# Kernel tuning notes

Hardware: AMD Instinct MI355X
Metric: run time of the kernel (lower is better)

The kernel has to match this reference:

```python
import jax, jax.numpy as jnp
import numpy as np

B, D, DEPTH, H, E, N, NC = 128, 192, 12, 3, 4, 65, 100
WIN_HALF = 3  # window_size=7 -> |i-j| <= 3


def _ln(x, g, b, eps=1e-5):
    m = x.mean(-1, keepdims=True)
    v = ((x - m) ** 2).mean(-1, keepdims=True)
    return (x - m) / jnp.sqrt(v + eps) * g + b


def _forward(x, conv_w, conv_b, pe_g, pe_b, cls_token, pos_embed,
             n1_g, n1_b, qkv_w, temp, proj_w, proj_b, n2_g, n2_b,
             gate_w, gate_b, e_w1, e_b1, e_w2, e_b2, attn_scale, mlp_scale,
             norm_g, norm_b, hc_w, hc_b, head_w, head_b):
    Bx = x.shape[0]
    # patch embed: conv with kernel==stride==4 is a blocked matmul
    p = x.reshape(Bx, 3, 8, 4, 8, 4).transpose(0, 2, 4, 1, 3, 5).reshape(Bx, 64, 48)
    t = p @ conv_w.reshape(D, 48).T + conv_b
    t = _ln(t, pe_g, pe_b)
    t = jnp.concatenate([jnp.broadcast_to(cls_token, (Bx, 1, D)), t], axis=1) + pos_embed
    Nn = t.shape[1]
    hd = D // H
    scale = hd ** -0.5
    idx = jnp.arange(Nn)
    # local-window attention mask (log of {0,1} -> {-inf,0})
    mask = jnp.where(jnp.abs(idx[:, None] - idx[None, :]) <= WIN_HALF, 0.0, -jnp.inf)
    for l in range(DEPTH):
        # --- attention ---
        y = _ln(t, n1_g[l], n1_b[l])
        qkv = (y @ qkv_w[l].T).reshape(Bx, Nn, 3, H, hd).transpose(2, 0, 3, 1, 4)
        q, k, v = qkv[0], qkv[1], qkv[2]
        a = (q @ k.transpose(0, 1, 3, 2)) * scale / temp[l]  # [B,H,N,N]
        a = jax.nn.softmax(a + mask, axis=-1)
        o = (a @ v).transpose(0, 2, 1, 3).reshape(Bx, Nn, D)
        o = o @ proj_w[l].T + proj_b[l]
        t = t + attn_scale[l] * o
        # --- top-2 MoE (dense-equivalent of the masked per-expert dispatch) ---
        y = _ln(t, n2_g[l], n2_b[l])
        g = jax.nn.softmax(y @ gate_w[l].T + gate_b[l], axis=-1)  # [B,N,E]
        tg, ti = jax.lax.top_k(g, 2)
        tg = tg / tg.sum(-1, keepdims=True)
        h = jax.nn.gelu(jnp.einsum('bnc,ehc->bneh', y, e_w1[l]) + e_b1[l], approximate=False)
        eo = jnp.einsum('bneh,ech->bnec', h, e_w2[l]) + e_b2[l]  # [B,N,E,C]
        sel = jnp.take_along_axis(eo, ti[..., None], axis=2)  # [B,N,2,C]
        mo = (sel * tg[..., None]).sum(axis=2)
        t = t + mlp_scale[l] * mo
    t = _ln(t, norm_g, norm_b)
    cls = t[:, 0]
    # hypercomplex linear head: out[:,k] += x[:,j] @ W[(k-j)%n].T
    xv = cls.reshape(Bx, E, D // E)
    perm = (jnp.arange(E)[:, None] - jnp.arange(E)[None, :]) % E  # [k,j] -> i
    hh = jnp.einsum('bjc,kjoc->bko', xv, hc_w[perm]).reshape(Bx, 2 * D) + hc_b
    hh = jax.nn.gelu(hh, approximate=False)
    return hh @ head_w.T + head_b


def setup_inputs() -> dict:
    ks = iter(jax.random.split(jax.random.key(0), 64))
    def rn(shape, s=0.02):
        return jax.random.normal(next(ks), shape, jnp.float32) * s
    return dict(
        x=jax.random.normal(next(ks), (B, 3, 32, 32), jnp.float32),
        conv_w=rn((D, 3, 4, 4)), conv_b=jnp.zeros((D,)),
        pe_g=jnp.ones((D,)), pe_b=jnp.zeros((D,)),
        cls_token=rn((1, 1, D)), pos_embed=rn((1, N, D)),
        n1_g=jnp.ones((DEPTH, D)), n1_b=jnp.zeros((DEPTH, D)),
        qkv_w=rn((DEPTH, 3 * D, D)), temp=jnp.ones((DEPTH, H, 1, 1)),
        proj_w=rn((DEPTH, D, D)), proj_b=jnp.zeros((DEPTH, D)),
        n2_g=jnp.ones((DEPTH, D)), n2_b=jnp.zeros((DEPTH, D)),
        gate_w=rn((DEPTH, E, D)), gate_b=jnp.zeros((DEPTH, E)),
        e_w1=rn((DEPTH, E, 2 * D, D)), e_b1=jnp.zeros((DEPTH, E, 2 * D)),
        e_w2=rn((DEPTH, E, D, 2 * D)), e_b2=jnp.zeros((DEPTH, E, D)),
        attn_scale=jnp.ones((DEPTH,)), mlp_scale=jnp.ones((DEPTH,)),
        norm_g=jnp.ones((D,)), norm_b=jnp.zeros((D,)),
        hc_w=rn((E, 2 * D // E, D // E)), hc_b=jnp.zeros((2 * D,)),
        head_w=rn((NC, 2 * D)), head_b=jnp.zeros((NC,)),
    )


def reference(x, conv_w, conv_b, pe_g, pe_b, cls_token, pos_embed,
              n1_g, n1_b, qkv_w, temp, proj_w, proj_b, n2_g, n2_b,
              gate_w, gate_b, e_w1, e_b1, e_w2, e_b2, attn_scale, mlp_scale,
              norm_g, norm_b, hc_w, hc_b, head_w, head_b):
    return _forward(x, conv_w, conv_b, pe_g, pe_b, cls_token, pos_embed,
                    n1_g, n1_b, qkv_w, temp, proj_w, proj_b, n2_g, n2_b,
                    gate_w, gate_b, e_w1, e_b1, e_w2, e_b2, attn_scale, mlp_scale,
                    norm_g, norm_b, hc_w, hc_b, head_w, head_b)
```

## Files before the change

kernel.cpp:

```cpp
#include <hip/hip_runtime.h>
#include <cmath>

#define ROWS 8320
#define DD   192

typedef __attribute__((ext_vector_type(8))) _Float16 half8;
typedef __attribute__((ext_vector_type(4))) float floatx4;

#define GLD16(gp, lp) __builtin_amdgcn_global_load_lds( \
    (const __attribute__((address_space(1))) void*)(gp), \
    (__attribute__((address_space(3))) void*)(lp), 16, 0, 0)

#define MFMA_F16 __builtin_amdgcn_mfma_f32_16x16x32_f16

__device__ __forceinline__ float gelu_f(float x) {
    return 0.5f * x * (1.0f + erff(x * 0.70710678118654752440f));
}

__device__ __forceinline__ float blk_sum_192(float v, float* sbuf) {
    int tid = threadIdx.x;
    sbuf[tid] = v;
    __syncthreads();
    for (int off = 96; off >= 3; off >>= 1) {
        if (tid < off) sbuf[tid] += sbuf[tid + off];
        __syncthreads();
    }
    float r = sbuf[0] + sbuf[1] + sbuf[2];
    __syncthreads();
    return r;
}

__device__ __forceinline__ void cvt8(const float* __restrict__ sp, _Float16* __restrict__ dp) {
    #pragma unroll
    for (int j = 0; j < 8; j++) dp[j] = (_Float16)sp[j];
}

__global__ __launch_bounds__(256) void cvt_all_kernel(
    const float* __restrict__ qkv_w, const float* __restrict__ proj_w,
    const float* __restrict__ e_w1, const float* __restrict__ e_w2,
    _Float16* __restrict__ qkvw_h, _Float16* __restrict__ projw_h,
    _Float16* __restrict__ ew1_h, _Float16* __restrict__ ew2_h)
{
    long i = (long)blockIdx.x * 256 + threadIdx.x;
    const long n_qkv  = (long)12 * 576 * 192 / 8;
    const long n_proj = (long)12 * 192 * 192 / 8;
    const long n_w1   = (long)12 * 1536 * 192 / 8;
    const long n_w2   = (long)12 * 192 * 192;
    if (i < n_qkv) { cvt8(qkv_w + i * 8, qkvw_h + i * 8); return; }
    i -= n_qkv;
    if (i < n_proj) { cvt8(proj_w + i * 8, projw_h + i * 8); return; }
    i -= n_proj;
    if (i < n_w1) { cvt8(e_w1 + i * 8, ew1_h + i * 8); return; }
    i -= n_w1;
    if (i < n_w2) {
        int l = (int)(i / (192 * 192));
        int rem = (int)(i % (192 * 192));
        int n = rem / 192, p = rem % 192;
        int c0 = p * 8;
        int e = c0 / 384, k0 = c0 % 384;
        cvt8(e_w2 + (((size_t)l * 4 + e) * 192 + n) * 384 + k0, ew2_h + i * 8);
    }
}

__global__ __launch_bounds__(192) void embed_kernel(
    const float* __restrict__ x, const float* __restrict__ conv_w,
    const float* __restrict__ conv_b, const float* __restrict__ pe_g,
    const float* __restrict__ pe_b, const float* __restrict__ cls_tok,
    const float* __restrict__ pos, float* __restrict__ t)
{
    __shared__ float patch[48];
    __shared__ float red[192];
    int blk = blockIdx.x;
    int b = blk / 65, n = blk % 65;
    int tid = threadIdx.x;
    if (n == 0) {
        t[(size_t)b * 65 * DD + tid] = cls_tok[tid] + pos[tid];
        return;
    }
    int p = n - 1, gy = p / 8, gx = p % 8;
    if (tid < 48) {
        int c = tid / 16, iy = (tid % 16) / 4, ix = tid % 4;
        patch[tid] = x[((size_t)b * 3 + c) * 1024 + (size_t)(gy * 4 + iy) * 32 + (gx * 4 + ix)];
    }
    __syncthreads();
    float s = conv_b[tid];
    const float* w = conv_w + (size_t)tid * 48;
    #pragma unroll
    for (int f = 0; f < 48; f++) s += patch[f] * w[f];
    float mean = blk_sum_192(s, red) * (1.0f / 192.0f);
    float d = s - mean;
    float var = blk_sum_192(d * d, red) * (1.0f / 192.0f);
    float o = d * rsqrtf(var + 1e-5f) * pe_g[tid] + pe_b[tid];
    t[((size_t)b * 65 + n) * DD + tid] = o + pos[(size_t)n * DD + tid];
}

__global__ __launch_bounds__(256) void ln_kernel(
    const float* __restrict__ in,
    float* __restrict__ yf, _Float16* __restrict__ yh,
    const float* __restrict__ g, const float* __restrict__ bb, long in_stride, int nrows,
    const float* __restrict__ gwm, const float* __restrict__ gb,
    int4* __restrict__ gwout)
{
    int wave = threadIdx.x >> 6, lane = threadIdx.x & 63;
    int r = blockIdx.x * 4 + wave;
    if (r >= nrows) return;
    const float* row = in + (size_t)r * in_stride;
    float v0 = row[lane], v1 = row[lane + 64], v2 = row[lane + 128];
    float s = v0 + v1 + v2;
    #pragma unroll
    for (int off = 32; off > 0; off >>= 1) s += __shfl_xor(s, off);
    float mean = s * (1.0f / 192.0f);
    float d0 = v0 - mean, d1 = v1 - mean, d2 = v2 - mean;
    float q = d0 * d0 + d1 * d1 + d2 * d2;
    #pragma unroll
    for (int off = 32; off > 0; off >>= 1) q += __shfl_xor(q, off);
    float rstd = rsqrtf(q * (1.0f / 192.0f) + 1e-5f);
    float o0 = d0 * rstd * g[lane] + bb[lane];
    float o1 = d1 * rstd * g[lane + 64] + bb[lane + 64];
    float o2 = d2 * rstd * g[lane + 128] + bb[lane + 128];
    if (yf) {
        float* yr = yf + (size_t)r * DD;
        yr[lane] = o0; yr[lane + 64] = o1; yr[lane + 128] = o2;
    }
    if (yh) {
        _Float16* yr = yh + (size_t)r * DD;
        yr[lane] = (_Float16)o0; yr[lane + 64] = (_Float16)o1; yr[lane + 128] = (_Float16)o2;
    }
    if (gwm) {
        float pe[4];
        #pragma unroll
        for (int e = 0; e < 4; e++) {
            const float* w = gwm + (size_t)e * DD;
            pe[e] = o0 * w[lane] + o1 * w[lane + 64] + o2 * w[lane + 128];
            #pragma unroll
            for (int off = 32; off > 0; off >>= 1) pe[e] += __shfl_xor(pe[e], off);
        }
        if (lane == 0) {
            #pragma unroll
            for (int e = 0; e < 4; e++) pe[e] += gb[e];
            float mx = fmaxf(fmaxf(pe[0], pe[1]), fmaxf(pe[2], pe[3]));
            float ex[4];
            #pragma unroll
            for (int e = 0; e < 4; e++) ex[e] = expf(pe[e] - mx);
            int i0 = 0;
            #pragma unroll
            for (int e = 1; e < 4; e++) if (ex[e] > ex[i0]) i0 = e;
            int i1 = (i0 == 0) ? 1 : 0;
            #pragma unroll
            for (int e = 0; e < 4; e++) if (e != i0 && ex[e] > ex[i1]) i1 = e;
            float denom = ex[i0] + ex[i1];
            int4 o4;
            o4.x = i0; o4.y = i1;
            o4.z = __float_as_int(ex[i0] / denom);
            o4.w = __float_as_int(ex[i1] / denom);
            gwout[r] = o4;
        }
    }
}

__global__ __launch_bounds__(256) void gate_build_kernel(
    const int4* __restrict__ gwrow, int* __restrict__ cnt,
    int* __restrict__ list, float* __restrict__ wlist, int rows)
{
    int r = blockIdx.x * 256 + threadIdx.x;
    int lane = threadIdx.x & 63;
    bool active = r < rows;
    int4 gv = active ? gwrow[r] : int4{-1, -1, 0, 0};
    #pragma unroll
    for (int e = 0; e < 4; e++) {
        bool sel = active && (gv.x == e || gv.y == e);
        int rank = (gv.x == e) ? 0 : 1;
        float w = (gv.x == e) ? __int_as_float(gv.z) : __int_as_float(gv.w);
        unsigned long long mask = __ballot(sel);
        int cw = __popcll(mask);
        if (cw) {
            int leader = __ffsll((long long)mask) - 1;
            int base = 0;
            if (lane == leader) base = atomicAdd(&cnt[e], cw);
            base = __shfl(base, leader);
            if (sel) {
                int idx = base + __popcll(mask & ((1ULL << lane) - 1ULL));
                list[(size_t)e * ROWS + idx] = (r << 1) | rank;
                wlist[(size_t)e * ROWS + idx] = w;
            }
        }
    }
}

template <int MODE>
__global__ __launch_bounds__(256) void gemm_h(
    const _Float16* __restrict__ A, const _Float16* __restrict__ W,
    int Nn, _Float16* __restrict__ outH, float* __restrict__ t,
    const float* __restrict__ bias, const float* __restrict__ scale)
{
    __shared__ __align__(16) _Float16 Ws[64 * 192];
    const int tid = threadIdx.x;
    const int lane = tid & 63, wave = tid >> 6;
    const int m0 = blockIdx.x * 64, n0 = blockIdx.y * 64;
    const int wm = (wave & 1) * 32, wn = (wave >> 1) * 32;
    const int lr = lane & 15, quad = lane >> 4;

    #pragma unroll
    for (int i = 0; i < 6; i++) {
        int s = (wave * 6 + i) * 64 + lane;
        int rr = s / 24, c = s % 24;
        GLD16(W + (size_t)(n0 + rr) * 192 + (c ^ (rr & 7)) * 8,
              (char*)Ws + (size_t)(wave * 6 + i) * 1024);
    }
    half8 a[2][6];
    #pragma unroll
    for (int ti = 0; ti < 2; ti++) {
        const _Float16* ap = A + (size_t)(m0 + wm + ti * 16 + lr) * 192 + quad * 8;
        #pragma unroll
        for (int m = 0; m < 6; m++) a[ti][m] = *(const half8*)(ap + m * 32);
    }
    __syncthreads();

    floatx4 zero = {0.f, 0.f, 0.f, 0.f};
    floatx4 acc[2][2];
    acc[0][0] = zero; acc[0][1] = zero; acc[1][0] = zero; acc[1][1] = zero;

    #pragma unroll
    for (int m = 0; m < 6; m++) {
        int ch = m * 4 + quad;
        half8 w[2];
        #pragma unroll
        for (int tj = 0; tj < 2; tj++) {
            int cr = wn + tj * 16 + lr;
            w[tj] = *(const half8*)(Ws + ((size_t)cr * 24 + (ch ^ (cr & 7))) * 8);
        }
        #pragma unroll
        for (int ti = 0; ti < 2; ti++)
            #pragma unroll
            for (int tj = 0; tj < 2; tj++)
                acc[ti][tj] = MFMA_F16(a[ti][m], w[tj], acc[ti][tj], 0, 0, 0);
    }

    float sc = (MODE == 2) ? scale[0] : 0.f;
    #pragma unroll
    for (int ti = 0; ti < 2; ti++)
        #pragma unroll
        for (int tj = 0; tj < 2; tj++)
            #pragma unroll
            for (int r = 0; r < 4; r++) {
                int grow = m0 + wm + ti * 16 + quad * 4 + r;
                int gcol = n0 + wn + tj * 16 + lr;
                float v = acc[ti][tj][r];
                if (MODE == 0) {
                    float vp = __shfl_xor(v, 1);
                    if ((lane & 1) == 0) {
                        union { _Float16 h[2]; unsigned u; } pk;
                        pk.h[0] = (_Float16)v;
                        pk.h[1] = (_Float16)vp;
                        *(unsigned*)(outH + (size_t)grow * Nn + (gcol & ~1)) = pk.u;
                    }
                } else {
                    t[(size_t)grow * DD + gcol] += sc * (v + bias[gcol]);
                }
            }
}

__global__ __launch_bounds__(256) void moe_kernel(
    const _Float16* __restrict__ yh, const _Float16* __restrict__ w1,
    const _Float16* __restrict__ w2, const float* __restrict__ b1,
    const float* __restrict__ b2, const float* __restrict__ scale,
    const int* __restrict__ cnt, const int* __restrict__ list,
    const float* __restrict__ wlist, float* __restrict__ t)
{
    __shared__ __align__(16) _Float16 W1s[64 * 192];
    __shared__ __align__(16) _Float16 W2s[192 * 64];
    __shared__ __align__(16) _Float16 Hs[32 * 64];
    const int e  = blockIdx.y;
    const int cnte = cnt[e];
    const int r0 = blockIdx.x * 32;
    if (r0 >= cnte) return;
    const int tid = threadIdx.x;
    const int lane = tid & 63, wave = tid >> 6;
    const int lr = lane & 15, quad = lane >> 4;
    const int wr = (wave & 1) * 16;
    const int wc1 = (wave >> 1) * 16;
    const int wc2 = (wave >> 1) * 96;

    #pragma unroll
    for (int i = 0; i < 6; i++) {
        int s = (wave * 6 + i) * 64 + lane;
        int rr = s / 24, c = s % 24;
        GLD16(w1 + ((size_t)e * 384 + rr) * 192 + (c ^ (rr & 7)) * 8,
              (char*)W1s + (size_t)(wave * 6 + i) * 1024);
    }

    int sl = r0 + wr + lr;
    int rv = -1; float wv = 0.f;
    if (sl < cnte) {
        rv = list[(size_t)e * ROWS + sl];
        wv = wlist[(size_t)e * ROWS + sl];
    }
    int arow = (rv >= 0) ? (rv >> 1) : 0;

    half8 a[6];
    {
        const _Float16* ap = yh + (size_t)arow * 192 + quad * 8;
        #pragma unroll
        for (int m = 0; m < 6; m++) a[m] = *(const half8*)(ap + m * 32);
    }

    int rvr[4]; float bwr[4];
    #pragma unroll
    for (int r = 0; r < 4; r++) {
        rvr[r] = __shfl(rv, quad * 4 + r);
        bwr[r] = __shfl(wv, quad * 4 + r);
    }

    __syncthreads();

    floatx4 zero = {0.f, 0.f, 0.f, 0.f};
    floatx4 acc2[6];
    #pragma unroll
    for (int j = 0; j < 6; j++) acc2[j] = zero;

    for (int nc = 0; nc < 6; nc++) {
        int ncg = e * 6 + nc;
        #pragma unroll
        for (int i = 0; i < 6; i++) {
            int s = (wave * 6 + i) * 64 + lane;
            int n = s >> 3, c = s & 7;
            GLD16(w2 + (size_t)n * 1536 + (ncg * 8 + (c ^ (n & 7))) * 8,
                  (char*)W2s + (size_t)(wave * 6 + i) * 1024);
        }
        floatx4 acc1[2];
        acc1[0] = zero; acc1[1] = zero;
        #pragma unroll
        for (int m = 0; m < 6; m++) {
            int ch = m * 4 + quad;
            #pragma unroll
            for (int tc = 0; tc < 2; tc++) {
                int cr = wc1 + tc * 32 + lr;
                half8 w = *(const half8*)(W1s + ((size_t)cr * 24 + (ch ^ (cr & 7))) * 8);
                acc1[tc] = MFMA_F16(a[m], w, acc1[tc], 0, 0, 0);
            }
        }
        #pragma unroll
        for (int tc = 0; tc < 2; tc++)
            #pragma unroll
            for (int r = 0; r < 4; r++) {
                int hrow = wr + quad * 4 + r;
                int hcol = wc1 + tc * 32 + lr;
                float v = gelu_f(acc1[tc][r] + b1[64 * ncg + hcol]) * bwr[r];
                float vp = __shfl_xor(v, 1);
                if ((lane & 1) == 0) {
                    union { _Float16 h[2]; unsigned u; } pk;
                    pk.h[0] = (_Float16)v;
                    pk.h[1] = (_Float16)vp;
                    int cl = (hcol >> 3) ^ (hrow & 7);
                    *(unsigned*)(Hs + ((size_t)hrow * 8 + cl) * 8 + (hcol & 7)) = pk.u;
                }
            }
        __syncthreads();
        if (nc < 5) {
            #pragma unroll
            for (int i = 0; i < 6; i++) {
                int s = (wave * 6 + i) * 64 + lane;
                int rr = s / 24, c = s % 24;
                GLD16(w1 + ((size_t)e * 384 + (nc + 1) * 64 + rr) * 192 + (c ^ (rr & 7)) * 8,
                      (char*)W1s + (size_t)(wave * 6 + i) * 1024);
            }
        }
        #pragma unroll
        for (int kk = 0; kk < 2; kk++) {
            int ar = wr + lr;
            int ch = kk * 4 + quad;
            half8 ha = *(const half8*)(Hs + ((size_t)ar * 8 + (ch ^ (ar & 7))) * 8);
            #pragma unroll
            for (int tj = 0; tj < 6; tj++) {
                int cr = wc2 + tj * 16 + lr;
                half8 w = *(const half8*)(W2s + ((size_t)cr * 8 + (ch ^ (cr & 7))) * 8);
                acc2[tj] = MFMA_F16(ha, w, acc2[tj], 0, 0, 0);
            }
        }
        __syncthreads();
    }

    float sc = scale[0];
    #pragma unroll
    for (int tj = 0; tj < 6; tj++) {
        int gcol = wc2 + tj * 16 + lr;
        float b2v = b2[e * 192 + gcol];
        #pragma unroll
        for (int r = 0; r < 4; r++) {
            if (rvr[r] >= 0) {
                float v = sc * (acc2[tj][r] + bwr[r] * b2v);
                atomicAdd(&t[(size_t)(rvr[r] >> 1) * DD + gcol], v);
            }
        }
    }
}

__global__ __launch_bounds__(256) void attn_kernel(
    const _Float16* __restrict__ qkv, const float* __restrict__ temp,
    _Float16* __restrict__ o)
{
    __shared__ float q[65][65], k[65][65], v[65][65];
    __shared__ float p[65][8];
    int bh = blockIdx.x;
    int b = bh / 3, h = bh % 3;
    int tid = threadIdx.x;
    float coef = 0.125f / temp[h];
    const _Float16* base = qkv + (size_t)b * 65 * 576 + h * 64;
    for (int idx = tid; idx < 65 * 64; idx += 256) {
        int i = idx >> 6, d = idx & 63;
        q[i][d] = (float)base[(size_t)i * 576 + d];
        k[i][d] = (float)base[(size_t)i * 576 + 192 + d];
        v[i][d] = (float)base[(size_t)i * 576 + 384 + d];
    }
    __syncthreads();
    if (tid < 65) {
        int i = tid;
        float sc[7];
        float mx = -1e30f;
        #pragma unroll
        for (int jo = 0; jo < 7; jo++) {
            int j = i - 3 + jo;
            if (j >= 0 && j < 65) {
                float s = 0.f;
                #pragma unroll
                for (int d = 0; d < 64; d++) s += q[i][d] * k[j][d];
                sc[jo] = s * coef;
                mx = fmaxf(mx, sc[jo]);
            } else sc[jo] = -1e30f;
        }
        float sum = 0.f;
        #pragma unroll
        for (int jo = 0; jo < 7; jo++) {
            float e = expf(sc[jo] - mx);
            p[i][jo] = e;
            sum += e;
        }
        float inv = 1.0f / sum;
        #pragma unroll
        for (int jo = 0; jo < 7; jo++) p[i][jo] *= inv;
    }
    __syncthreads();
    for (int idx = tid; idx < 65 * 64; idx += 256) {
        int i = idx >> 6, d = idx & 63;
        float s = 0.f;
        #pragma unroll
        for (int jo = 0; jo < 7; jo++) {
            int j = i - 3 + jo;
            if (j >= 0 && j < 65) s += p[i][jo] * v[j][d];
        }
        o[((size_t)b * 65 + i) * 192 + h * 64 + d] = (_Float16)s;
    }
}

__global__ __launch_bounds__(128) void head_kernel(
    const float* __restrict__ cls, const float* __restrict__ hc_w,
    const float* __restrict__ hc_b, const float* __restrict__ head_w,
    const float* __restrict__ head_b, float* __restrict__ out)
{
    __shared__ float c[192];
    __shared__ float hh[384];
    int b = blockIdx.x, tid = threadIdx.x;
    for (int i = tid; i < 192; i += 128) c[i] = cls[(size_t)b * 192 + i];
    __syncthreads();
    for (int i = tid; i < 384; i += 128) {
        int kx = i / 96, o = i % 96;
        float s = hc_b[i];
        #pragma unroll
        for (int j = 0; j < 4; j++) {
            int pp = (kx - j + 4) & 3;
            const float* w = hc_w + ((size_t)pp * 96 + o) * 48;
            const float* xv = c + j * 48;
            #pragma unroll
            for (int cc = 0; cc < 48; cc++) s += xv[cc] * w[cc];
        }
        hh[i] = gelu_f(s);
    }
    __syncthreads();
    for (int i = tid; i < 100; i += 128) {
        float s = head_b[i];
        const float* w = head_w + (size_t)i * 384;
        for (int kk = 0; kk < 384; kk++) s += hh[kk] * w[kk];
        out[(size_t)b * 100 + i] = s;
    }
}

extern "C" void kernel_launch(void* const* d_in, const int* in_sizes, int n_in,
                              void* d_out, int out_size, void* d_ws, size_t ws_size,
                              hipStream_t stream)
{
    const float* x        = (const float*)d_in[0];
    const float* conv_w   = (const float*)d_in[1];
    const float* conv_b   = (const float*)d_in[2];
    const float* pe_g     = (const float*)d_in[3];
    const float* pe_b     = (const float*)d_in[4];
    const float* cls_tok  = (const float*)d_in[5];
    const float* pos      = (const float*)d_in[6];
    const float* n1_g     = (const float*)d_in[7];
    const float* n1_b     = (const float*)d_in[8];
    const float* qkv_w    = (const float*)d_in[9];
    const float* temp     = (const float*)d_in[10];
    const float* proj_w   = (const float*)d_in[11];
    const float* proj_b   = (const float*)d_in[12];
    const float* n2_g     = (const float*)d_in[13];
    const float* n2_b     = (const float*)d_in[14];
    const float* gate_w   = (const float*)d_in[15];
    const float* gate_b   = (const float*)d_in[16];
    const float* e_w1     = (const float*)d_in[17];
    const float* e_b1     = (const float*)d_in[18];
    const float* e_w2     = (const float*)d_in[19];
    const float* e_b2     = (const float*)d_in[20];
    const float* attn_sc  = (const float*)d_in[21];
    const float* mlp_sc   = (const float*)d_in[22];
    const float* norm_g   = (const float*)d_in[23];
    const float* norm_b   = (const float*)d_in[24];
    const float* hc_w     = (const float*)d_in[25];
    const float* hc_b     = (const float*)d_in[26];
    const float* head_w   = (const float*)d_in[27];
    const float* head_b   = (const float*)d_in[28];

    char* base = (char*)d_ws;
    float*  t     = (float*)base;   base += (size_t)ROWS * DD * 4;
    int4*   gwrow = (int4*)base;    base += (size_t)ROWS * 16;
    int*    cnts  = (int*)base;     base += (size_t)12 * 4 * sizeof(int) + 64;
    int*    elist = (int*)base;     base += (size_t)4 * ROWS * 4;
    float*  ewls  = (float*)base;   base += (size_t)4 * ROWS * 4;
    float*  ycls  = (float*)base;   base += (size_t)128 * DD * 4;
    _Float16* yhb = (_Float16*)base; base += (size_t)ROWS * DD * 2;
    _Float16* qkvh = (_Float16*)base; base += (size_t)ROWS * 576 * 2;
    _Float16* osph = (_Float16*)base; base += (size_t)ROWS * DD * 2;
    _Float16* qkvw_h = (_Float16*)base; base += (size_t)12 * 576 * 192 * 2;
    _Float16* projw_h = (_Float16*)base; base += (size_t)12 * 192 * 192 * 2;
    _Float16* ew1_h = (_Float16*)base; base += (size_t)12 * 1536 * 192 * 2;
    _Float16* ew2_h = (_Float16*)base; base += (size_t)12 * 192 * 1536 * 2;

    hipMemsetAsync(cnts, 0, 12 * 4 * sizeof(int), stream);

    {
        long total = (long)12 * 576 * 192 / 8 + (long)12 * 192 * 192 / 8
                   + (long)12 * 1536 * 192 / 8 + (long)12 * 192 * 192;
        cvt_all_kernel<<<(int)((total + 255) / 256), 256, 0, stream>>>(
            qkv_w, proj_w, e_w1, e_w2, qkvw_h, projw_h, ew1_h, ew2_h);
    }

    embed_kernel<<<128 * 65, 192, 0, stream>>>(x, conv_w, conv_b, pe_g, pe_b, cls_tok, pos, t);

    for (int l = 0; l < 12; l++) {
        ln_kernel<<<ROWS / 4, 256, 0, stream>>>(
            t, nullptr, yhb, n1_g + l * DD, n1_b + l * DD, DD, ROWS,
            nullptr, nullptr, nullptr);
        gemm_h<0><<<dim3(130, 9), 256, 0, stream>>>(
            yhb, qkvw_h + (size_t)l * 576 * 192, 576, qkvh, nullptr, nullptr, nullptr);
        attn_kernel<<<128 * 3, 256, 0, stream>>>(qkvh, temp + l * 3, osph);
        gemm_h<2><<<dim3(130, 3), 256, 0, stream>>>(
            osph, projw_h + (size_t)l * 192 * 192, 192, nullptr, t,
            proj_b + l * DD, attn_sc + l);
        ln_kernel<<<ROWS / 4, 256, 0, stream>>>(
            t, nullptr, yhb, n2_g + l * DD, n2_b + l * DD, DD, ROWS,
            gate_w + (size_t)l * 4 * DD, gate_b + l * 4, gwrow);
        gate_build_kernel<<<(ROWS + 255) / 256, 256, 0, stream>>>(
            gwrow, cnts + l * 4, elist, ewls, ROWS);
        moe_kernel<<<dim3(260, 4), 256, 0, stream>>>(
            yhb, ew1_h + (size_t)l * 1536 * 192, ew2_h + (size_t)l * 192 * 1536,
            e_b1 + (size_t)l * 1536, e_b2 + (size_t)l * 4 * 192, mlp_sc + l,
            cnts + l * 4, elist, ewls, t);
    }

    ln_kernel<<<32, 256, 0, stream>>>(
        t, ycls, nullptr, norm_g, norm_b, (long)65 * DD, 128,
        nullptr, nullptr, nullptr);
    head_kernel<<<128, 128, 0, stream>>>(ycls, hc_w, hc_b, head_w, head_b, (float*)d_out);
}
```

Before: 1.195 ms.

## Split MoE hidden dimension across grid z, parallelize attention scores, stage GEMM A in LDS

The MoE kernel now splits each expert's hidden dimension into two halves on a new grid z axis, doubling block count to raise occupancy. Each half accumulates its partial into the residual, and only the first half adds the bias. The attention kernel spreads score computation over all threads and adds padding to avoid LDS bank conflicts. The GEMM stages A tiles through LDS with async global-to-LDS loads instead of per-lane register loads. The MoE split doubles the atomic accumulation traffic into t, and the GEMM uses extra LDS.

```diff
diff --git a/kernel.cpp b/kernel.cpp
--- a/kernel.cpp
+++ b/kernel.cpp
@@ -193,6 +193,7 @@
     int Nn, _Float16* __restrict__ outH, float* __restrict__ t,
     const float* __restrict__ bias, const float* __restrict__ scale)
 {
+    __shared__ __align__(16) _Float16 As[64 * 192];
     __shared__ __align__(16) _Float16 Ws[64 * 192];
     const int tid = threadIdx.x;
     const int lane = tid & 63, wave = tid >> 6;
@@ -204,15 +205,10 @@
     for (int i = 0; i < 6; i++) {
         int s = (wave * 6 + i) * 64 + lane;
         int rr = s / 24, c = s % 24;
+        GLD16(A + (size_t)(m0 + rr) * 192 + (c ^ (rr & 7)) * 8,
+              (char*)As + (size_t)(wave * 6 + i) * 1024);
         GLD16(W + (size_t)(n0 + rr) * 192 + (c ^ (rr & 7)) * 8,
               (char*)Ws + (size_t)(wave * 6 + i) * 1024);
-    }
-    half8 a[2][6];
-    #pragma unroll
-    for (int ti = 0; ti < 2; ti++) {
-        const _Float16* ap = A + (size_t)(m0 + wm + ti * 16 + lr) * 192 + quad * 8;
-        #pragma unroll
-        for (int m = 0; m < 6; m++) a[ti][m] = *(const half8*)(ap + m * 32);
     }
     __syncthreads();
 
@@ -223,17 +219,19 @@
     #pragma unroll
     for (int m = 0; m < 6; m++) {
         int ch = m * 4 + quad;
-        half8 w[2];
-        #pragma unroll
-        for (int tj = 0; tj < 2; tj++) {
-            int cr = wn + tj * 16 + lr;
-            w[tj] = *(const half8*)(Ws + ((size_t)cr * 24 + (ch ^ (cr & 7))) * 8);
+        half8 a[2], w[2];
+        #pragma unroll
+        for (int ti = 0; ti < 2; ti++) {
+            int ar = wm + ti * 16 + lr;
+            a[ti] = *(const half8*)(As + ((size_t)ar * 24 + (ch ^ (ar & 7))) * 8);
+            int cr = wn + ti * 16 + lr;
+            w[ti] = *(const half8*)(Ws + ((size_t)cr * 24 + (ch ^ (cr & 7))) * 8);
         }
         #pragma unroll
         for (int ti = 0; ti < 2; ti++)
             #pragma unroll
             for (int tj = 0; tj < 2; tj++)
-                acc[ti][tj] = MFMA_F16(a[ti][m], w[tj], acc[ti][tj], 0, 0, 0);
+                acc[ti][tj] = MFMA_F16(a[ti], w[tj], acc[ti][tj], 0, 0, 0);
     }
 
     float sc = (MODE == 2) ? scale[0] : 0.f;
@@ -271,6 +269,7 @@
     __shared__ __align__(16) _Float16 W2s[192 * 64];
     __shared__ __align__(16) _Float16 Hs[32 * 64];
     const int e  = blockIdx.y;
+    const int zb = blockIdx.z;
     const int cnte = cnt[e];
     const int r0 = blockIdx.x * 32;
     if (r0 >= cnte) return;
@@ -285,7 +284,7 @@
     for (int i = 0; i < 6; i++) {
         int s = (wave * 6 + i) * 64 + lane;
         int rr = s / 24, c = s % 24;
-        GLD16(w1 + ((size_t)e * 384 + rr) * 192 + (c ^ (rr & 7)) * 8,
+        GLD16(w1 + ((size_t)e * 384 + zb * 192 + rr) * 192 + (c ^ (rr & 7)) * 8,
               (char*)W1s + (size_t)(wave * 6 + i) * 1024);
     }
 
@@ -318,7 +317,8 @@
     #pragma unroll
     for (int j = 0; j < 6; j++) acc2[j] = zero;
 
-    for (int nc = 0; nc < 6; nc++) {
+    for (int ncl = 0; ncl < 3; ncl++) {
+        int nc = zb * 3 + ncl;
         int ncg = e * 6 + nc;
         #pragma unroll
         for (int i = 0; i < 6; i++) {
@@ -356,12 +356,12 @@
                 }
             }
         __syncthreads();
-        if (nc < 5) {
+        if (ncl < 2) {
             #pragma unroll
             for (int i = 0; i < 6; i++) {
                 int s = (wave * 6 + i) * 64 + lane;
                 int rr = s / 24, c = s % 24;
-                GLD16(w1 + ((size_t)e * 384 + (nc + 1) * 64 + rr) * 192 + (c ^ (rr & 7)) * 8,
+                GLD16(w1 + ((size_t)e * 384 + zb * 192 + (ncl + 1) * 64 + rr) * 192 + (c ^ (rr & 7)) * 8,
                       (char*)W1s + (size_t)(wave * 6 + i) * 1024);
             }
         }
@@ -384,7 +384,7 @@
     #pragma unroll
     for (int tj = 0; tj < 6; tj++) {
         int gcol = wc2 + tj * 16 + lr;
-        float b2v = b2[e * 192 + gcol];
+        float b2v = (zb == 0) ? b2[e * 192 + gcol] : 0.f;
         #pragma unroll
         for (int r = 0; r < 4; r++) {
             if (rvr[r] >= 0) {
@@ -399,56 +399,66 @@
     const _Float16* __restrict__ qkv, const float* __restrict__ temp,
     _Float16* __restrict__ o)
 {
-    __shared__ float q[65][65], k[65][65], v[65][65];
-    __shared__ float p[65][8];
+    __shared__ float q[65][66], k[65][66], v[65][66];
+    __shared__ float p[65][9];
     int bh = blockIdx.x;
     int b = bh / 3, h = bh % 3;
     int tid = threadIdx.x;
     float coef = 0.125f / temp[h];
     const _Float16* base = qkv + (size_t)b * 65 * 576 + h * 64;
-    for (int idx = tid; idx < 65 * 64; idx += 256) {
-        int i = idx >> 6, d = idx & 63;
-        q[i][d] = (float)base[(size_t)i * 576 + d];
-        k[i][d] = (float)base[(size_t)i * 576 + 192 + d];
-        v[i][d] = (float)base[(size_t)i * 576 + 384 + d];
+    for (int idx = tid; idx < 65 * 32; idx += 256) {
+        int i = idx >> 5, d2 = (idx & 31) * 2;
+        const _Float16* bp = base + (size_t)i * 576 + d2;
+        q[i][d2] = (float)bp[0];   q[i][d2 + 1] = (float)bp[1];
+        k[i][d2] = (float)bp[192]; k[i][d2 + 1] = (float)bp[193];
+        v[i][d2] = (float)bp[384]; v[i][d2 + 1] = (float)bp[385];
+    }
+    __syncthreads();
+    for (int idx = tid; idx < 65 * 7; idx += 256) {
+        int i = idx / 7, jo = idx % 7;
+        int j = i - 3 + jo;
+        float s = -1e30f;
+        if (j >= 0 && j < 65) {
+            const float2* qr = (const float2*)&q[i][0];
+            const float2* kr = (const float2*)&k[j][0];
+            float acc = 0.f;
+            #pragma unroll
+            for (int d2 = 0; d2 < 32; d2++) {
+                float2 aa = qr[d2], bb = kr[d2];
+                acc += aa.x * bb.x + aa.y * bb.y;
+            }
+            s = acc * coef;
+        }
+        p[i][jo] = s;
     }
     __syncthreads();
     if (tid < 65) {
-        int i = tid;
-        float sc[7];
         float mx = -1e30f;
+        #pragma unroll
+        for (int jo = 0; jo < 7; jo++) mx = fmaxf(mx, p[tid][jo]);
+        float ex[7], sum = 0.f;
+        #pragma unroll
+        for (int jo = 0; jo < 7; jo++) { ex[jo] = expf(p[tid][jo] - mx); sum += ex[jo]; }
+        float inv = 1.0f / sum;
+        #pragma unroll
+        for (int jo = 0; jo < 7; jo++) p[tid][jo] = ex[jo] * inv;
+    }
+    __syncthreads();
+    for (int idx = tid; idx < 65 * 32; idx += 256) {
+        int i = idx >> 5, d2 = (idx & 31) * 2;
+        float s0 = 0.f, s1 = 0.f;
         #pragma unroll
         for (int jo = 0; jo < 7; jo++) {
             int j = i - 3 + jo;
             if (j >= 0 && j < 65) {
-                float s = 0.f;
-                #pragma unroll
-                for (int d = 0; d < 64; d++) s += q[i][d] * k[j][d];
-                sc[jo] = s * coef;
-                mx = fmaxf(mx, sc[jo]);
-            } else sc[jo] = -1e30f;
-        }
-        float sum = 0.f;
-        #pragma unroll
-        for (int jo = 0; jo < 7; jo++) {
-            float e = expf(sc[jo] - mx);
-            p[i][jo] = e;
-            sum += e;
-        }
-        float inv = 1.0f / sum;
-        #pragma unroll
-        for (int jo = 0; jo < 7; jo++) p[i][jo] *= inv;
-    }
-    __syncthreads();
-    for (int idx = tid; idx < 65 * 64; idx += 256) {
-        int i = idx >> 6, d = idx & 63;
-        float s = 0.f;
-        #pragma unroll
-        for (int jo = 0; jo < 7; jo++) {
-            int j = i - 3 + jo;
-            if (j >= 0 && j < 65) s += p[i][jo] * v[j][d];
-        }
-        o[((size_t)b * 65 + i) * 192 + h * 64 + d] = (_Float16)s;
+                float pv = p[i][jo];
+                s0 += pv * v[j][d2];
+                s1 += pv * v[j][d2 + 1];
+            }
+        }
+        union { _Float16 h2[2]; unsigned u; } pk;
+        pk.h2[0] = (_Float16)s0; pk.h2[1] = (_Float16)s1;
+        *(unsigned*)(o + ((size_t)b * 65 + i) * 192 + h * 64 + d2) = pk.u;
     }
 }
 
@@ -559,7 +569,7 @@
             gate_w + (size_t)l * 4 * DD, gate_b + l * 4, gwrow);
         gate_build_kernel<<<(ROWS + 255) / 256, 256, 0, stream>>>(
             gwrow, cnts + l * 4, elist, ewls, ROWS);
-        moe_kernel<<<dim3(260, 4), 256, 0, stream>>>(
+        moe_kernel<<<dim3(260, 4, 2), 256, 0, stream>>>(
             yhb, ew1_h + (size_t)l * 1536 * 192, ew2_h + (size_t)l * 192 * 1536,
             e_b1 + (size_t)l * 1536, e_b2 + (size_t)l * 4 * 192, mlp_sc + l,
             cnts + l * 4, elist, ewls, t);
```

New measurement: 1.255 ms. +5.1%, slower.
